# Kernel optimization log

Hardware: AMD Instinct MI355X
Metric: run time of the kernel (lower is better)

## Reference

```python
import jax, jax.numpy as jnp
import numpy as np

N_NODE = 100000
N_EDGE = 1600000
IN_DIM = 128
HID = [64, 64]
OUT_DIM = 32
NUM_GRAPHS = 256


def setup_inputs() -> dict:
    key = jax.random.key(0)
    ks = jax.random.split(key, 12)
    x = jax.random.normal(ks[0], (N_NODE, IN_DIM), dtype=jnp.float32)
    senders = jax.random.randint(ks[1], (N_EDGE,), 0, N_NODE, dtype=jnp.int32)
    receivers = jax.random.randint(ks[2], (N_EDGE,), 0, N_NODE, dtype=jnp.int32)
    batch = jnp.sort(jax.random.randint(ks[3], (N_NODE,), 0, NUM_GRAPHS, dtype=jnp.int32))
    # Dense params for the 3 GCN layers (Glorot-ish scaling)
    def dense(k, din, dout):
        return jax.random.normal(k, (din, dout), dtype=jnp.float32) / np.sqrt(din)
    W1 = dense(ks[4], IN_DIM, HID[0]); b1 = jnp.zeros((HID[0],), jnp.float32)
    W2 = dense(ks[5], HID[0], HID[1]); b2 = jnp.zeros((HID[1],), jnp.float32)
    W3 = dense(ks[6], HID[1], OUT_DIM); b3 = jnp.zeros((OUT_DIM,), jnp.float32)
    return {"x": x, "W1": W1, "b1": b1, "W2": W2, "b2": b2, "W3": W3, "b3": b3,
            "senders": senders, "receivers": receivers, "batch": batch,
            "num_graphs": NUM_GRAPHS}


def _gcn_layer(x, W, b, senders, receivers, n_node):
    # Dense transform
    x = x @ W + b  # [N, dout]
    ones = jnp.ones(senders.shape[0], dtype=x.dtype)
    sender_deg = jax.ops.segment_sum(ones, senders, n_node)      # out-degree
    receiver_deg = jax.ops.segment_sum(ones, receivers, n_node)  # in-degree
    # symmetric normalization: D^{-1/2} A D^{-1/2}
    x = x * jax.lax.rsqrt(jnp.maximum(sender_deg, 1.0))[:, None]
    x = jax.ops.segment_sum(x[senders], receivers, n_node)       # gather + scatter-sum
    x = x * jax.lax.rsqrt(jnp.maximum(receiver_deg, 1.0))[:, None]
    return x


def reference(x, W1, b1, W2, b2, W3, b3, senders, receivers, batch, num_graphs):
    n_node = x.shape[0]
    x = jax.nn.relu(_gcn_layer(x, W1, b1, senders, receivers, n_node))
    x = jax.nn.relu(_gcn_layer(x, W2, b2, senders, receivers, n_node))
    x = _gcn_layer(x, W3, b3, senders, receivers, n_node)
    # graph-level sum pooling
    return jax.ops.segment_sum(x, batch, num_graphs)  # [num_graphs, OUT_DIM]
```

## Files before the change

### kernel.cpp

```cpp
#include <hip/hip_runtime.h>
#include <hip/hip_bf16.h>

#define N_NODE   100000
#define N_EDGE   1600000
#define IN_DIM   128
#define HID1     64
#define HID2     64
#define OUT_DIM  32
#define NUM_GRAPHS 256

#define NBUCK    782
#define BBLK     500
#define EPB      3200
#define STAGE_CAP 4096

typedef unsigned int uint;
typedef unsigned short ushort_t;
typedef short bf16x8 __attribute__((ext_vector_type(8)));
typedef float f32x4 __attribute__((ext_vector_type(4)));

__device__ __forceinline__ float bflo(uint p) { return __uint_as_float(p << 16); }
__device__ __forceinline__ float bfhi(uint p) { return __uint_as_float(p & 0xFFFF0000u); }
__device__ __forceinline__ uint bfpack(float a, float b) {
    uint ua = __float_as_uint(a), ub = __float_as_uint(b);
    ua = (ua + 0x7FFFu + ((ua >> 16) & 1u)) >> 16;
    ub = (ub + 0x7FFFu + ((ub >> 16) & 1u)) & 0xFFFF0000u;
    return ua | ub;
}
__device__ __forceinline__ ushort_t bf16r(float f) {
    uint ua = __float_as_uint(f);
    return (ushort_t)((ua + 0x7FFFu + ((ua >> 16) & 1u)) >> 16);
}


__global__ __launch_bounds__(256)
void k_count(const int2* __restrict__ snd2, const int2* __restrict__ rcv2,
             int* __restrict__ degS, int* __restrict__ cntA) {
    __shared__ int cnt[NBUCK];
    const int t = threadIdx.x, blk = blockIdx.x;
    for (int i = t; i < NBUCK; i += 256) cnt[i] = 0;
    __syncthreads();
    const int base2 = blk * (EPB / 2);
    for (int i = 0; i < 7; ++i) {
        int local2 = i * 256 + t;
        if (local2 < EPB / 2) {
            int2 r = rcv2[base2 + local2];
            int2 s = snd2[base2 + local2];
            atomicAdd(&cnt[r.x >> 7], 1);
            atomicAdd(&cnt[r.y >> 7], 1);
            atomicAdd(&degS[s.x], 1);
            atomicAdd(&degS[s.y], 1);
        }
    }
    __syncthreads();
    for (int i = t; i < NBUCK; i += 256) cntA[blk * NBUCK + i] = cnt[i];
}

__global__ __launch_bounds__(256)
void k_scanb(int* __restrict__ cntA, int* __restrict__ bucketTotal) {
    const int b = blockIdx.x, t = threadIdx.x, lane = t & 63, wave = t >> 6;
    __shared__ int sW[4];
    int carry = 0;
    for (int k = 0; k < 2; ++k) {
        int idx = k * 256 + t;
        int v = (idx < BBLK) ? cntA[idx * NBUCK + b] : 0;
        int inc = v;
        #pragma unroll
        for (int o = 1; o < 64; o <<= 1) { int n = __shfl_up(inc, o); if (lane >= o) inc += n; }
        if (lane == 63) sW[wave] = inc;
        __syncthreads();
        int wOff = 0;
        for (int w = 0; w < wave; ++w) wOff += sW[w];
        int tot = sW[0] + sW[1] + sW[2] + sW[3];
        int excl = carry + wOff + inc - v;
        if (idx < BBLK) cntA[idx * NBUCK + b] = excl;
        carry += tot;
        __syncthreads();
    }
    if (t == 0) bucketTotal[b] = carry;
}

__global__ __launch_bounds__(256)
void k_scanB(const int* __restrict__ bucketTotal, int* __restrict__ bucketBase) {
    const int t = threadIdx.x, lane = t & 63, wave = t >> 6;
    __shared__ int sW[4];
    int carry = 0;
    for (int k = 0; k < 4; ++k) {
        int idx = k * 256 + t;
        int v = (idx < NBUCK) ? bucketTotal[idx] : 0;
        int inc = v;
        #pragma unroll
        for (int o = 1; o < 64; o <<= 1) { int n = __shfl_up(inc, o); if (lane >= o) inc += n; }
        if (lane == 63) sW[wave] = inc;
        __syncthreads();
        int wOff = 0;
        for (int w = 0; w < wave; ++w) wOff += sW[w];
        int tot = sW[0] + sW[1] + sW[2] + sW[3];
        int excl = carry + wOff + inc - v;
        if (idx < NBUCK) bucketBase[idx] = excl;
        carry += tot;
        __syncthreads();
    }
    if (t == 0) bucketBase[NBUCK] = carry;
}

__global__ __launch_bounds__(256)
void k_place(const int2* __restrict__ snd2, const int2* __restrict__ rcv2,
             const int* __restrict__ colOff, const int* __restrict__ bucketBase,
             uint* __restrict__ binned) {
    __shared__ int cur[NBUCK];
    const int t = threadIdx.x, blk = blockIdx.x;
    for (int i = t; i < NBUCK; i += 256) cur[i] = 0;
    __syncthreads();
    const int base2 = blk * (EPB / 2);
    for (int i = 0; i < 7; ++i) {
        int local2 = i * 256 + t;
        if (local2 < EPB / 2) {
            int2 r = rcv2[base2 + local2];
            int2 s = snd2[base2 + local2];
            int b0 = r.x >> 7, b1 = r.y >> 7;
            int l0 = atomicAdd(&cur[b0], 1);
            binned[bucketBase[b0] + colOff[blk * NBUCK + b0] + l0] = ((uint)s.x << 7) | (uint)(r.x & 127);
            int l1 = atomicAdd(&cur[b1], 1);
            binned[bucketBase[b1] + colOff[blk * NBUCK + b1] + l1] = ((uint)s.y << 7) | (uint)(r.y & 127);
        }
    }
}

__global__ __launch_bounds__(256)
void k_local(const uint* __restrict__ binned, const int* __restrict__ bucketBase,
             const int* __restrict__ degS,
             int* __restrict__ rowptr, float* __restrict__ normS, float* __restrict__ normR,
             int* __restrict__ sortedSrc) {
    __shared__ uint staged[STAGE_CAP];
    __shared__ int cnt[128], excl[128], cur[128];
    const int b = blockIdx.x, t = threadIdx.x;
    const int e0 = bucketBase[b], e1 = bucketBase[b + 1], m = e1 - e0;
    if (t < 128) { cnt[t] = 0; cur[t] = 0; }
    __syncthreads();
    for (int i = t; i < m; i += 256) {
        uint v = binned[e0 + i];
        if (i < STAGE_CAP) staged[i] = v;
        atomicAdd(&cnt[v & 127u], 1);
    }
    __syncthreads();
    if (t < 64) {
        int v0 = cnt[t], v1 = cnt[64 + t];
        int i0 = v0;
        #pragma unroll
        for (int o = 1; o < 64; o <<= 1) { int n = __shfl_up(i0, o); if (t >= o) i0 += n; }
        excl[t] = i0 - v0;
        int tot0 = __shfl(i0, 63);
        int i1 = v1;
        #pragma unroll
        for (int o = 1; o < 64; o <<= 1) { int n = __shfl_up(i1, o); if (t >= o) i1 += n; }
        excl[64 + t] = tot0 + i1 - v1;
    }
    __syncthreads();
    if (t < 128) {
        int node = b * 128 + t;
        if (node < N_NODE) {
            rowptr[node] = e0 + excl[t];
            normR[node] = rsqrtf(fmaxf((float)cnt[t], 1.0f));
            normS[node] = rsqrtf(fmaxf((float)degS[node], 1.0f));
        }
    }
    if (b == NBUCK - 1 && t == 0) rowptr[N_NODE] = e1;
    for (int i = t; i < m; i += 256) {
        uint v = (i < STAGE_CAP) ? staged[i] : binned[e0 + i];
        int n7 = (int)(v & 127u);
        int lpos = atomicAdd(&cur[n7], 1);
        sortedSrc[e0 + excl[n7] + lpos] = (int)(v >> 7);
    }
}


__global__ __launch_bounds__(256)
void k_prepw(const float* __restrict__ W1, const float* __restrict__ W2,
             const float* __restrict__ W3,
             ushort_t* __restrict__ Wt1, ushort_t* __restrict__ Wt2,
             ushort_t* __restrict__ Wt3) {
    int i = blockIdx.x * 256 + threadIdx.x;
    if (i < 8192) {
        int col = i >> 7, k = i & 127;
        Wt1[i] = bf16r(W1[k * 64 + col]);
    } else if (i < 12288) {
        int j = i - 8192; int col = j >> 6, k = j & 63;
        Wt2[j] = bf16r(W2[k * 64 + col]);
    } else if (i < 14336) {
        int j = i - 12288; int col = j >> 6, k = j & 63;
        Wt3[j] = bf16r(W3[k * 32 + col]);
    }
}


template<int K, int N, bool F32IN>
__global__ __launch_bounds__(256)
void k_mgemm(const void* __restrict__ Xv, const ushort_t* __restrict__ Wt,
             const float* __restrict__ bias, const float* __restrict__ normS,
             uint* __restrict__ Y2) {
    __shared__ uint WL[N * K / 2];
    const int tid = threadIdx.x, wave = tid >> 6, lane = tid & 63;
    const uint* Wg = (const uint*)Wt;
    for (int i = tid; i < N * K / 2; i += 256) {
        int col = i / (K / 2);
        WL[i ^ ((col & 7) << 2)] = Wg[i];
    }
    const int m0 = blockIdx.x * 64 + wave * 16;
    const int arow = m0 + (lane & 15);
    const int asrc = (arow < N_NODE) ? arow : 0;
    const int koff = (lane >> 4) * 8;
    bf16x8 afr[K / 32];
    if (F32IN) {
        const float* Xf = (const float*)Xv + (size_t)asrc * K + koff;
        #pragma unroll
        for (int s = 0; s < K / 32; ++s) {
            float4 u = *(const float4*)(Xf + 32 * s);
            float4 v = *(const float4*)(Xf + 32 * s + 4);
            union { uint u4[4]; bf16x8 v8; } c;
            c.u4[0] = bfpack(u.x, u.y); c.u4[1] = bfpack(u.z, u.w);
            c.u4[2] = bfpack(v.x, v.y); c.u4[3] = bfpack(v.z, v.w);
            afr[s] = c.v8;
        }
    } else {
        const uint* Xp = (const uint*)Xv + (size_t)asrc * (K / 2) + (koff >> 1);
        #pragma unroll
        for (int s = 0; s < K / 32; ++s) {
            uint2 q0 = *(const uint2*)(Xp + 16 * s);
            uint2 q1 = *(const uint2*)(Xp + 16 * s + 2);
            union { uint u4[4]; bf16x8 v8; } c;
            c.u4[0] = q0.x; c.u4[1] = q0.y; c.u4[2] = q1.x; c.u4[3] = q1.y;
            afr[s] = c.v8;
        }
    }
    __syncthreads();
    f32x4 acc[N / 16];
    #pragma unroll
    for (int t = 0; t < N / 16; ++t) acc[t] = (f32x4){0.f, 0.f, 0.f, 0.f};
    #pragma unroll
    for (int s = 0; s < K / 32; ++s) {
        #pragma unroll
        for (int t = 0; t < N / 16; ++t) {
            int col = t * 16 + (lane & 15);
            int word = (col * (K / 2) + s * 16 + (koff >> 1)) ^ ((col & 7) << 2);
            bf16x8 bfr = *(const bf16x8*)&WL[word];
            acc[t] = __builtin_amdgcn_mfma_f32_16x16x32_bf16(afr[s], bfr, acc[t], 0, 0, 0);
        }
    }
    const int r0 = m0 + (lane >> 4) * 4;
    float ns[4];
    #pragma unroll
    for (int i = 0; i < 4; ++i) ns[i] = (r0 + i < N_NODE) ? normS[r0 + i] : 0.f;
    #pragma unroll
    for (int t = 0; t < N / 16; ++t) {
        int col = t * 16 + (lane & 15);
        float bv = bias[col];
        #pragma unroll
        for (int i = 0; i < 4; ++i) {
            float v = (acc[t][i] + bv) * ns[i];
            float w = __shfl_down(v, 1);
            if ((lane & 1) == 0 && r0 + i < N_NODE)
                Y2[(size_t)(r0 + i) * (N / 2) + (col >> 1)] = bfpack(v, w);
        }
    }
}


template<int F, bool RELU>
__global__ __launch_bounds__(256)
void k_agg(const uint* __restrict__ H2, const int* __restrict__ rowptr,
           const int* __restrict__ srcs, const float* __restrict__ normR,
           uint* __restrict__ Y2) {
    const int node = (blockIdx.x * 256 + threadIdx.x) >> 6;
    const int lane = threadIdx.x & 63;
    const int F2 = F / 2;
    const int PE = 64 / F2;
    const int sub = lane / F2;
    const int fj = lane % F2;
    const int start = rowptr[node], end = rowptr[node + 1];
    float a0 = 0.0f, a1 = 0.0f;
    int e = start + sub;
    for (; e + 3 * PE < end; e += 4 * PE) {
        int s0 = srcs[e], s1 = srcs[e + PE], s2 = srcs[e + 2 * PE], s3 = srcs[e + 3 * PE];
        uint p0 = H2[s0 * F2 + fj];
        uint p1 = H2[s1 * F2 + fj];
        uint p2 = H2[s2 * F2 + fj];
        uint p3 = H2[s3 * F2 + fj];
        a0 += bflo(p0); a1 += bfhi(p0);
        a0 += bflo(p1); a1 += bfhi(p1);
        a0 += bflo(p2); a1 += bfhi(p2);
        a0 += bflo(p3); a1 += bfhi(p3);
    }
    for (; e < end; e += PE) {
        uint p = H2[srcs[e] * F2 + fj];
        a0 += bflo(p); a1 += bfhi(p);
    }
    if (PE == 4) { a0 += __shfl_xor(a0, 16); a1 += __shfl_xor(a1, 16); }
    a0 += __shfl_xor(a0, 32); a1 += __shfl_xor(a1, 32);
    if (lane < F2) {
        float nr = normR[node];
        float r0 = a0 * nr, r1 = a1 * nr;
        if (RELU) { r0 = fmaxf(r0, 0.0f); r1 = fmaxf(r1, 0.0f); }
        Y2[node * F2 + fj] = bfpack(r0, r1);
    }
}


__global__ __launch_bounds__(256)
void k_pool(const uint* __restrict__ H2, const int* __restrict__ batch,
            float* __restrict__ out) {
    const int wid = (blockIdx.x * 256 + threadIdx.x) >> 6;
    const int lane = threadIdx.x & 63;
    const int NPW = (N_NODE + 1023) / 1024;
    int n0 = wid * NPW, n1 = min(n0 + NPW, N_NODE);
    const int p = lane >> 4, fj = lane & 15;
    float a0 = 0.0f, a1 = 0.0f;
    int gCur = -1;
    for (int n = n0 + p; n < n1; n += 4) {
        int g = batch[n];
        uint v = H2[n * 16 + fj];
        if (g != gCur) {
            if (gCur >= 0) {
                atomicAdd(&out[gCur * OUT_DIM + 2 * fj], a0);
                atomicAdd(&out[gCur * OUT_DIM + 2 * fj + 1], a1);
            }
            gCur = g; a0 = bflo(v); a1 = bfhi(v);
        } else {
            a0 += bflo(v); a1 += bfhi(v);
        }
    }
    if (gCur >= 0) {
        atomicAdd(&out[gCur * OUT_DIM + 2 * fj], a0);
        atomicAdd(&out[gCur * OUT_DIM + 2 * fj + 1], a1);
    }
}


extern "C" void kernel_launch(void* const* d_in, const int* in_sizes, int n_in,
                              void* d_out, int out_size, void* d_ws, size_t ws_size,
                              hipStream_t stream) {
    const float* x   = (const float*)d_in[0];
    const float* W1  = (const float*)d_in[1];
    const float* b1  = (const float*)d_in[2];
    const float* W2  = (const float*)d_in[3];
    const float* b2  = (const float*)d_in[4];
    const float* W3  = (const float*)d_in[5];
    const float* b3  = (const float*)d_in[6];
    const int* snd   = (const int*)d_in[7];
    const int* rcv   = (const int*)d_in[8];
    const int* batch = (const int*)d_in[9];
    float* out = (float*)d_out;

    char* ws = (char*)d_ws;
    size_t off = 0;
    auto carve = [&](size_t bytes) { char* p = ws + off; off += (bytes + 15) & ~size_t(15); return p; };
    int*   degS        = (int*)  carve(N_NODE * 4);
    int*   cntA        = (int*)  carve((size_t)BBLK * NBUCK * 4);
    int*   bucketTotal = (int*)  carve(NBUCK * 4);
    int*   bucketBase  = (int*)  carve((NBUCK + 1) * 4);
    int*   rowptr      = (int*)  carve((N_NODE + 1) * 4);
    uint*  binned      = (uint*) carve((size_t)N_EDGE * 4);
    int*   sortedSrc   = (int*)  carve((size_t)N_EDGE * 4);
    float* normS       = (float*)carve(N_NODE * 4);
    float* normR       = (float*)carve(N_NODE * 4);
    ushort_t* Wt1      = (ushort_t*)carve(8192 * 2);
    ushort_t* Wt2      = (ushort_t*)carve(4096 * 2);
    ushort_t* Wt3      = (ushort_t*)carve(2048 * 2);
    uint*  bufA        = (uint*) carve((size_t)N_NODE * 32 * 4);
    uint*  bufB        = (uint*) carve((size_t)N_NODE * 32 * 4);

    hipMemsetAsync(d_ws, 0, N_NODE * 4, stream);
    hipMemsetAsync(d_out, 0, NUM_GRAPHS * OUT_DIM * 4, stream);

    k_prepw<<<56, 256, 0, stream>>>(W1, W2, W3, Wt1, Wt2, Wt3);
    k_count<<<BBLK, 256, 0, stream>>>((const int2*)snd, (const int2*)rcv, degS, cntA);
    k_scanb<<<NBUCK, 256, 0, stream>>>(cntA, bucketTotal);
    k_scanB<<<1, 256, 0, stream>>>(bucketTotal, bucketBase);
    k_place<<<BBLK, 256, 0, stream>>>((const int2*)snd, (const int2*)rcv, cntA, bucketBase, binned);
    k_local<<<NBUCK, 256, 0, stream>>>(binned, bucketBase, degS, rowptr, normS, normR, sortedSrc);

    const int AGG_B = (N_NODE * 64 + 255) / 256;
    const int GB = (N_NODE + 63) / 64;

    k_mgemm<IN_DIM, HID1, true><<<GB, 256, 0, stream>>>(x, Wt1, b1, normS, bufA);
    k_agg<HID1, true><<<AGG_B, 256, 0, stream>>>(bufA, rowptr, sortedSrc, normR, bufB);

    k_mgemm<HID1, HID2, false><<<GB, 256, 0, stream>>>(bufB, Wt2, b2, normS, bufA);
    k_agg<HID2, true><<<AGG_B, 256, 0, stream>>>(bufA, rowptr, sortedSrc, normR, bufB);

    k_mgemm<HID2, OUT_DIM, false><<<GB, 256, 0, stream>>>(bufB, Wt3, b3, normS, bufA);
    k_agg<OUT_DIM, false><<<AGG_B, 256, 0, stream>>>(bufA, rowptr, sortedSrc, normR, bufB);

    k_pool<<<256, 256, 0, stream>>>(bufB, batch, out);
}
```

Before: 419.2 us.

## Compute sender degrees via bucketed binning instead of global atomics

New measurement: 380.1 us. 1.1x faster.

```diff
diff --git a/kernel.cpp b/kernel.cpp
--- a/kernel.cpp
+++ b/kernel.cpp
@@ -15,6 +15,7 @@
 #define STAGE_CAP 4096
 
 typedef unsigned int uint;
+typedef unsigned char uchar;
 typedef unsigned short ushort_t;
 typedef short bf16x8 __attribute__((ext_vector_type(8)));
 typedef float f32x4 __attribute__((ext_vector_type(4)));
@@ -35,10 +36,11 @@
 
 __global__ __launch_bounds__(256)
 void k_count(const int2* __restrict__ snd2, const int2* __restrict__ rcv2,
-             int* __restrict__ degS, int* __restrict__ cntA) {
-    __shared__ int cnt[NBUCK];
+             int* __restrict__ cntRA, int* __restrict__ cntSA) {
+    __shared__ int cntR[NBUCK];
+    __shared__ int cntS[NBUCK];
     const int t = threadIdx.x, blk = blockIdx.x;
-    for (int i = t; i < NBUCK; i += 256) cnt[i] = 0;
+    for (int i = t; i < NBUCK; i += 256) { cntR[i] = 0; cntS[i] = 0; }
     __syncthreads();
     const int base2 = blk * (EPB / 2);
     for (int i = 0; i < 7; ++i) {
@@ -46,19 +48,27 @@
         if (local2 < EPB / 2) {
             int2 r = rcv2[base2 + local2];
             int2 s = snd2[base2 + local2];
-            atomicAdd(&cnt[r.x >> 7], 1);
-            atomicAdd(&cnt[r.y >> 7], 1);
-            atomicAdd(&degS[s.x], 1);
-            atomicAdd(&degS[s.y], 1);
-        }
-    }
-    __syncthreads();
-    for (int i = t; i < NBUCK; i += 256) cntA[blk * NBUCK + i] = cnt[i];
-}
-
-__global__ __launch_bounds__(256)
-void k_scanb(int* __restrict__ cntA, int* __restrict__ bucketTotal) {
-    const int b = blockIdx.x, t = threadIdx.x, lane = t & 63, wave = t >> 6;
+            atomicAdd(&cntR[r.x >> 7], 1);
+            atomicAdd(&cntR[r.y >> 7], 1);
+            atomicAdd(&cntS[s.x >> 7], 1);
+            atomicAdd(&cntS[s.y >> 7], 1);
+        }
+    }
+    __syncthreads();
+    for (int i = t; i < NBUCK; i += 256) {
+        cntRA[blk * NBUCK + i] = cntR[i];
+        cntSA[blk * NBUCK + i] = cntS[i];
+    }
+}
+
+__global__ __launch_bounds__(256)
+void k_scanb(int* __restrict__ cntRA, int* __restrict__ cntSA,
+             int* __restrict__ rTotal, int* __restrict__ sTotal) {
+    const int which = blockIdx.x / NBUCK;
+    const int b = blockIdx.x % NBUCK;
+    int* cntA = which ? cntSA : cntRA;
+    int* total = which ? sTotal : rTotal;
+    const int t = threadIdx.x, lane = t & 63, wave = t >> 6;
     __shared__ int sW[4];
     int carry = 0;
     for (int k = 0; k < 2; ++k) {
@@ -77,17 +87,20 @@
         carry += tot;
         __syncthreads();
     }
-    if (t == 0) bucketTotal[b] = carry;
-}
-
-__global__ __launch_bounds__(256)
-void k_scanB(const int* __restrict__ bucketTotal, int* __restrict__ bucketBase) {
+    if (t == 0) total[b] = carry;
+}
+
+__global__ __launch_bounds__(256)
+void k_scanB(const int* __restrict__ rTotal, const int* __restrict__ sTotal,
+             int* __restrict__ rBase, int* __restrict__ sBase) {
+    const int* total = blockIdx.x ? sTotal : rTotal;
+    int* base = blockIdx.x ? sBase : rBase;
     const int t = threadIdx.x, lane = t & 63, wave = t >> 6;
     __shared__ int sW[4];
     int carry = 0;
     for (int k = 0; k < 4; ++k) {
         int idx = k * 256 + t;
-        int v = (idx < NBUCK) ? bucketTotal[idx] : 0;
+        int v = (idx < NBUCK) ? total[idx] : 0;
         int inc = v;
         #pragma unroll
         for (int o = 1; o < 64; o <<= 1) { int n = __shfl_up(inc, o); if (lane >= o) inc += n; }
@@ -97,20 +110,22 @@
         for (int w = 0; w < wave; ++w) wOff += sW[w];
         int tot = sW[0] + sW[1] + sW[2] + sW[3];
         int excl = carry + wOff + inc - v;
-        if (idx < NBUCK) bucketBase[idx] = excl;
+        if (idx < NBUCK) base[idx] = excl;
         carry += tot;
         __syncthreads();
     }
-    if (t == 0) bucketBase[NBUCK] = carry;
+    if (t == 0) base[NBUCK] = carry;
 }
 
 __global__ __launch_bounds__(256)
 void k_place(const int2* __restrict__ snd2, const int2* __restrict__ rcv2,
-             const int* __restrict__ colOff, const int* __restrict__ bucketBase,
-             uint* __restrict__ binned) {
-    __shared__ int cur[NBUCK];
+             const int* __restrict__ rColOff, const int* __restrict__ sColOff,
+             const int* __restrict__ rBase, const int* __restrict__ sBase,
+             uint* __restrict__ binned, uchar* __restrict__ sBin) {
+    __shared__ int curR[NBUCK];
+    __shared__ int curS[NBUCK];
     const int t = threadIdx.x, blk = blockIdx.x;
-    for (int i = t; i < NBUCK; i += 256) cur[i] = 0;
+    for (int i = t; i < NBUCK; i += 256) { curR[i] = 0; curS[i] = 0; }
     __syncthreads();
     const int base2 = blk * (EPB / 2);
     for (int i = 0; i < 7; ++i) {
@@ -119,29 +134,38 @@
             int2 r = rcv2[base2 + local2];
             int2 s = snd2[base2 + local2];
             int b0 = r.x >> 7, b1 = r.y >> 7;
-            int l0 = atomicAdd(&cur[b0], 1);
-            binned[bucketBase[b0] + colOff[blk * NBUCK + b0] + l0] = ((uint)s.x << 7) | (uint)(r.x & 127);
-            int l1 = atomicAdd(&cur[b1], 1);
-            binned[bucketBase[b1] + colOff[blk * NBUCK + b1] + l1] = ((uint)s.y << 7) | (uint)(r.y & 127);
-        }
-    }
-}
-
-__global__ __launch_bounds__(256)
-void k_local(const uint* __restrict__ binned, const int* __restrict__ bucketBase,
-             const int* __restrict__ degS,
+            int l0 = atomicAdd(&curR[b0], 1);
+            binned[rBase[b0] + rColOff[blk * NBUCK + b0] + l0] = ((uint)s.x << 7) | (uint)(r.x & 127);
+            int l1 = atomicAdd(&curR[b1], 1);
+            binned[rBase[b1] + rColOff[blk * NBUCK + b1] + l1] = ((uint)s.y << 7) | (uint)(r.y & 127);
+            int c0 = s.x >> 7, c1 = s.y >> 7;
+            int m0 = atomicAdd(&curS[c0], 1);
+            sBin[sBase[c0] + sColOff[blk * NBUCK + c0] + m0] = (uchar)(s.x & 127);
+            int m1 = atomicAdd(&curS[c1], 1);
+            sBin[sBase[c1] + sColOff[blk * NBUCK + c1] + m1] = (uchar)(s.y & 127);
+        }
+    }
+}
+
+__global__ __launch_bounds__(256)
+void k_local(const uint* __restrict__ binned, const uchar* __restrict__ sBin,
+             const int* __restrict__ rBase, const int* __restrict__ sBase,
              int* __restrict__ rowptr, float* __restrict__ normS, float* __restrict__ normR,
              int* __restrict__ sortedSrc) {
     __shared__ uint staged[STAGE_CAP];
-    __shared__ int cnt[128], excl[128], cur[128];
+    __shared__ int cnt[128], excl[128], cur[128], cntS2[128];
     const int b = blockIdx.x, t = threadIdx.x;
-    const int e0 = bucketBase[b], e1 = bucketBase[b + 1], m = e1 - e0;
-    if (t < 128) { cnt[t] = 0; cur[t] = 0; }
+    const int e0 = rBase[b], e1 = rBase[b + 1], m = e1 - e0;
+    const int s0 = sBase[b], s1 = sBase[b + 1], ms = s1 - s0;
+    if (t < 128) { cnt[t] = 0; cur[t] = 0; cntS2[t] = 0; }
     __syncthreads();
     for (int i = t; i < m; i += 256) {
         uint v = binned[e0 + i];
         if (i < STAGE_CAP) staged[i] = v;
         atomicAdd(&cnt[v & 127u], 1);
+    }
+    for (int i = t; i < ms; i += 256) {
+        atomicAdd(&cntS2[(int)sBin[s0 + i]], 1);
     }
     __syncthreads();
     if (t < 64) {
@@ -162,7 +186,7 @@
         if (node < N_NODE) {
             rowptr[node] = e0 + excl[t];
             normR[node] = rsqrtf(fmaxf((float)cnt[t], 1.0f));
-            normS[node] = rsqrtf(fmaxf((float)degS[node], 1.0f));
+            normS[node] = rsqrtf(fmaxf((float)cntS2[t], 1.0f));
         }
     }
     if (b == NBUCK - 1 && t == 0) rowptr[N_NODE] = e1;
@@ -354,12 +378,15 @@
     char* ws = (char*)d_ws;
     size_t off = 0;
     auto carve = [&](size_t bytes) { char* p = ws + off; off += (bytes + 15) & ~size_t(15); return p; };
-    int*   degS        = (int*)  carve(N_NODE * 4);
-    int*   cntA        = (int*)  carve((size_t)BBLK * NBUCK * 4);
-    int*   bucketTotal = (int*)  carve(NBUCK * 4);
-    int*   bucketBase  = (int*)  carve((NBUCK + 1) * 4);
+    int*   cntRA       = (int*)  carve((size_t)BBLK * NBUCK * 4);
+    int*   cntSA       = (int*)  carve((size_t)BBLK * NBUCK * 4);
+    int*   rTotal      = (int*)  carve(NBUCK * 4);
+    int*   sTotal      = (int*)  carve(NBUCK * 4);
+    int*   rBase       = (int*)  carve((NBUCK + 1) * 4);
+    int*   sBase       = (int*)  carve((NBUCK + 1) * 4);
     int*   rowptr      = (int*)  carve((N_NODE + 1) * 4);
     uint*  binned      = (uint*) carve((size_t)N_EDGE * 4);
+    uchar* sBin        = (uchar*)carve((size_t)N_EDGE);
     int*   sortedSrc   = (int*)  carve((size_t)N_EDGE * 4);
     float* normS       = (float*)carve(N_NODE * 4);
     float* normR       = (float*)carve(N_NODE * 4);
@@ -369,15 +396,16 @@
     uint*  bufA        = (uint*) carve((size_t)N_NODE * 32 * 4);
     uint*  bufB        = (uint*) carve((size_t)N_NODE * 32 * 4);
 
-    hipMemsetAsync(d_ws, 0, N_NODE * 4, stream);
     hipMemsetAsync(d_out, 0, NUM_GRAPHS * OUT_DIM * 4, stream);
 
     k_prepw<<<56, 256, 0, stream>>>(W1, W2, W3, Wt1, Wt2, Wt3);
-    k_count<<<BBLK, 256, 0, stream>>>((const int2*)snd, (const int2*)rcv, degS, cntA);
-    k_scanb<<<NBUCK, 256, 0, stream>>>(cntA, bucketTotal);
-    k_scanB<<<1, 256, 0, stream>>>(bucketTotal, bucketBase);
-    k_place<<<BBLK, 256, 0, stream>>>((const int2*)snd, (const int2*)rcv, cntA, bucketBase, binned);
-    k_local<<<NBUCK, 256, 0, stream>>>(binned, bucketBase, degS, rowptr, normS, normR, sortedSrc);
+    k_count<<<BBLK, 256, 0, stream>>>((const int2*)snd, (const int2*)rcv, cntRA, cntSA);
+    k_scanb<<<2 * NBUCK, 256, 0, stream>>>(cntRA, cntSA, rTotal, sTotal);
+    k_scanB<<<2, 256, 0, stream>>>(rTotal, sTotal, rBase, sBase);
+    k_place<<<BBLK, 256, 0, stream>>>((const int2*)snd, (const int2*)rcv, cntRA, cntSA,
+                                      rBase, sBase, binned, sBin);
+    k_local<<<NBUCK, 256, 0, stream>>>(binned, sBin, rBase, sBase,
+                                       rowptr, normS, normR, sortedSrc);
 
     const int AGG_B = (N_NODE * 64 + 255) / 256;
     const int GB = (N_NODE + 63) / 64;
```
